# Kernel optimization log

Hardware: AMD Instinct MI355X
Metric: run time of the kernel (lower is better)

The kernel has to match this reference:

```python
import jax, jax.numpy as jnp
import numpy as np
import math

N_GRAPHS = 25
NODES_PER = 2000
N = N_GRAPHS * NODES_PER      # 50000 total nodes
E = 800000                    # total edges
D = 128                       # hidden = out_dim
VOCAB = 30                    # node_len
NLAYERS = 4                   # gcn_num_layers


def setup_inputs() -> dict:
    key = jax.random.key(0)
    ks = jax.random.split(key, 16)
    labels = jax.random.randint(ks[0], (N,), 0, VOCAB)
    src = jax.random.randint(ks[1], (E,), 0, N)
    dst = jax.random.randint(ks[2], (E,), 0, N)
    # true permutations per graph (as the torch code assumes)
    perms = jax.vmap(lambda k: jax.random.permutation(k, NODES_PER))(
        jax.random.split(ks[3], N_GRAPHS))
    s = 0.02
    emb = jax.random.normal(ks[4], (VOCAB, D)) * s
    Ws = jax.random.normal(ks[5], (NLAYERS, D, D)) * s
    bs = jnp.zeros((NLAYERS, D))
    # MLPReadout(D, D) with L=2: D -> D//2 -> D//4 -> D
    w1 = jax.random.normal(ks[6], (D, D // 2)) * s
    b1 = jnp.zeros((D // 2,))
    w2 = jax.random.normal(ks[7], (D // 2, D // 4)) * s
    b2 = jnp.zeros((D // 4,))
    w3 = jax.random.normal(ks[8], (D // 4, D)) * s
    b3 = jnp.zeros((D,))
    return {"labels": labels, "src": src, "dst": dst, "perms": perms,
            "emb": emb, "Ws": Ws, "bs": bs,
            "w1": w1, "b1": b1, "w2": w2, "b2": b2, "w3": w3, "b3": b3}


def _pos_encoding(perms):
    # sinusoidal table [NODES_PER, D]; position starts at 1 per the torch code
    pos = (jnp.arange(NODES_PER, dtype=jnp.float32) + 1.0)[:, None]       # [n,1]
    div = jnp.exp(jnp.arange(0, D, 2, dtype=jnp.float32)
                  * (-math.log(10000.0) / D))                              # [D/2]
    ang = pos * div                                                        # [n,D/2]
    table = jnp.stack([jnp.sin(ang), jnp.cos(ang)], axis=-1).reshape(NODES_PER, D)
    # pes[i][perm_i] = table  (scatter rows per graph)
    pe = jax.vmap(lambda p: jnp.zeros((NODES_PER, D), jnp.float32).at[p].set(table))(perms)
    return pe.reshape(N, D)


def reference(labels, src, dst, perms, emb, Ws, bs, w1, b1, w2, b2, w3, b3):
    h = emb[labels]                                   # embedding lookup [N,D]
    h = h + _pos_encoding(perms)

    ones = jnp.ones((E,), jnp.float32)
    deg_out = jnp.maximum(jax.ops.segment_sum(ones, src, num_segments=N), 1.0)
    deg_in = jnp.maximum(jax.ops.segment_sum(ones, dst, num_segments=N), 1.0)
    isq_src = deg_out ** -0.5                         # DGL GraphConv norm='both'
    isq_dst = deg_in ** -0.5

    for l in range(NLAYERS):
        hn = h * isq_src[:, None]
        m = jax.ops.segment_sum(hn[src], dst, num_segments=N)  # gather-scatter
        m = m * isq_dst[:, None]
        out = jax.nn.relu(m @ Ws[l] + bs[l])
        h = out + h                                   # residual (all dims equal)

    # MLPReadout: D -> D//2 -> D//4 -> D
    x = jax.nn.relu(h @ w1 + b1)
    x = jax.nn.relu(x @ w2 + b2)
    return x @ w3 + b3                                # [N, D]
```

## Files before the change

### kernel.cpp

```cpp
#include <hip/hip_runtime.h>

#define N_NODES 50000
#define N_EDGES 800000
#define D 128
#define NLAYERS 4
#define NODES_PER 2000
#define CAP 64
#define NB_BUILD 3125
#define NB_INIT 25000

typedef __attribute__((ext_vector_type(8))) short bf16x8;
typedef __attribute__((ext_vector_type(4))) float f32x4;

__device__ inline unsigned rne16(float f) {
    unsigned u = __float_as_uint(f);
    return (u + 0x7fffu + ((u >> 16) & 1u)) >> 16;
}
__device__ inline unsigned pack_bf2(float a, float b) {
    return rne16(a) | (rne16(b) << 16);
}
__device__ inline float4 bf4_to_f4(uint2 v) {
    float4 r;
    r.x = __uint_as_float(v.x << 16);
    r.y = __uint_as_float(v.x & 0xffff0000u);
    r.z = __uint_as_float(v.y << 16);
    r.w = __uint_as_float(v.y & 0xffff0000u);
    return r;
}

__global__ void build_init_kernel(const int* __restrict__ src, const int* __restrict__ dst,
                                  int* __restrict__ cursor, int* __restrict__ cnt_out_rep,
                                  unsigned short* __restrict__ bucket,
                                  const int* __restrict__ labels, const int* __restrict__ perms,
                                  const float* __restrict__ emb, float* __restrict__ h,
                                  const float* __restrict__ Ws, unsigned short* __restrict__ Wt,
                                  const float* __restrict__ w1, unsigned short* __restrict__ w1t,
                                  const float* __restrict__ w2, unsigned short* __restrict__ w2t,
                                  const float* __restrict__ w3, unsigned short* __restrict__ w3t) {
    int b = blockIdx.x;
    if (b < NB_BUILD) {
        int e = b * 256 + threadIdx.x;
        if (e < N_EDGES) {
            int s = src[e], d = dst[e];
            atomicAdd(&cnt_out_rep[(b & 3) * N_NODES + s], 1);
            int pos = atomicAdd(&cursor[d], 1);
            if (pos < CAP) bucket[d * CAP + pos] = (unsigned short)s;
        }
    } else if (b < NB_BUILD + NB_INIT) {
        int j = (b - NB_BUILD) * 2 + (threadIdx.x >> 7);
        int d = threadIdx.x & 127;
        int g = j / NODES_PER;
        int i = j - g * NODES_PER;
        int node = g * NODES_PER + perms[j];
        int k = d >> 1;
        float ang = (float)(i + 1) * expf((float)(2 * k) * (-9.210340371976184f / 128.0f));
        float pe = (d & 1) ? cosf(ang) : sinf(ang);
        h[node * D + d] = emb[labels[node] * D + d] + pe;
    } else {
        int tb = b - NB_BUILD - NB_INIT;
        if (tb < NLAYERS) {
            const float* W = Ws + (size_t)tb * D * D;
            unsigned short* T = Wt + (size_t)tb * D * D;
            for (int i = threadIdx.x; i < D * D; i += 256) {
                int k = i >> 7, n = i & 127;
                T[n * D + k] = (unsigned short)rne16(W[i]);
            }
        } else if (tb == NLAYERS) {
            for (int i = threadIdx.x; i < 128 * 64; i += 256) {
                int k = i >> 6, n = i & 63;
                w1t[n * 128 + k] = (unsigned short)rne16(w1[i]);
            }
        } else if (tb == NLAYERS + 1) {
            for (int i = threadIdx.x; i < 64 * 32; i += 256) {
                int k = i >> 5, n = i & 31;
                w2t[n * 64 + k] = (unsigned short)rne16(w2[i]);
            }
        } else {
            for (int i = threadIdx.x; i < 32 * 128; i += 256) {
                int k = i >> 7, n = i & 127;
                w3t[n * 32 + k] = (unsigned short)rne16(w3[i]);
            }
        }
    }
}

__global__ void finalize_kernel(const int* __restrict__ cursor,
                                const int* __restrict__ cnt_out_rep,
                                float* __restrict__ isq_src, float* __restrict__ isq_dst) {
    int i = blockIdx.x * 256 + threadIdx.x;
    if (i < N_NODES) {
        int co = cnt_out_rep[i] + cnt_out_rep[N_NODES + i] +
                 cnt_out_rep[2 * N_NODES + i] + cnt_out_rep[3 * N_NODES + i];
        isq_src[i] = rsqrtf((float)max(co, 1));
        isq_dst[i] = rsqrtf((float)max(cursor[i], 1));
    }
}

__global__ void hs16_kernel(const float* __restrict__ h, const float* __restrict__ isq_src,
                            unsigned short* __restrict__ hs16) {
    int gid = blockIdx.x * 256 + threadIdx.x;
    int row = gid >> 4;
    int c8 = (gid & 15) * 8;
    float s = isq_src[row];
    size_t idx = (size_t)row * D + c8;
    float4 v0 = *(const float4*)&h[idx];
    float4 v1 = *(const float4*)&h[idx + 4];
    uint4 o;
    o.x = pack_bf2(v0.x * s, v0.y * s);
    o.y = pack_bf2(v0.z * s, v0.w * s);
    o.z = pack_bf2(v1.x * s, v1.y * s);
    o.w = pack_bf2(v1.z * s, v1.w * s);
    *(uint4*)&hs16[idx] = o;
}

__global__ __launch_bounds__(256) void aggregate_kernel(const unsigned short* __restrict__ hs16,
        const int* __restrict__ cursor, const unsigned short* __restrict__ bucket,
        const float* __restrict__ isq_dst, unsigned short* __restrict__ m16) {
    int node = blockIdx.x * 4 + (threadIdx.x >> 6);
    int lane = threadIdx.x & 63;
    int q = lane >> 4;
    int col = lane & 15;
    int deg = min(cursor[node], CAP);
    int start = node * CAP;
    int end = start + deg;
    const unsigned short* hb = hs16 + col * 8;
    float a[8] = {0.f, 0.f, 0.f, 0.f, 0.f, 0.f, 0.f, 0.f};

    int e = start;
    for (; e + 8 <= end; e += 8) {
        int s0 = bucket[e + q];
        int s1 = bucket[e + 4 + q];
        uint4 v0 = *(const uint4*)&hb[s0 * D];
        uint4 v1 = *(const uint4*)&hb[s1 * D];
        float4 f0 = bf4_to_f4(make_uint2(v0.x, v0.y));
        float4 f1 = bf4_to_f4(make_uint2(v0.z, v0.w));
        float4 f2 = bf4_to_f4(make_uint2(v1.x, v1.y));
        float4 f3 = bf4_to_f4(make_uint2(v1.z, v1.w));
        a[0] += f0.x; a[1] += f0.y; a[2] += f0.z; a[3] += f0.w;
        a[4] += f1.x; a[5] += f1.y; a[6] += f1.z; a[7] += f1.w;
        a[0] += f2.x; a[1] += f2.y; a[2] += f2.z; a[3] += f2.w;
        a[4] += f3.x; a[5] += f3.y; a[6] += f3.z; a[7] += f3.w;
    }
    if (e + 4 <= end) {
        int s0 = bucket[e + q];
        uint4 v0 = *(const uint4*)&hb[s0 * D];
        float4 f0 = bf4_to_f4(make_uint2(v0.x, v0.y));
        float4 f1 = bf4_to_f4(make_uint2(v0.z, v0.w));
        a[0] += f0.x; a[1] += f0.y; a[2] += f0.z; a[3] += f0.w;
        a[4] += f1.x; a[5] += f1.y; a[6] += f1.z; a[7] += f1.w;
        e += 4;
    }
    int r = end - e;
    if (q < r) {
        int s0 = bucket[e + q];
        uint4 v0 = *(const uint4*)&hb[s0 * D];
        float4 f0 = bf4_to_f4(make_uint2(v0.x, v0.y));
        float4 f1 = bf4_to_f4(make_uint2(v0.z, v0.w));
        a[0] += f0.x; a[1] += f0.y; a[2] += f0.z; a[3] += f0.w;
        a[4] += f1.x; a[5] += f1.y; a[6] += f1.z; a[7] += f1.w;
    }
#pragma unroll
    for (int i = 0; i < 8; ++i) {
        a[i] += __shfl_xor(a[i], 16, 64);
        a[i] += __shfl_xor(a[i], 32, 64);
    }
    if (q == 0) {
        float wd = isq_dst[node];
        uint4 o;
        o.x = pack_bf2(a[0] * wd, a[1] * wd);
        o.y = pack_bf2(a[2] * wd, a[3] * wd);
        o.z = pack_bf2(a[4] * wd, a[5] * wd);
        o.w = pack_bf2(a[6] * wd, a[7] * wd);
        *(uint4*)&m16[node * D + col * 8] = o;
    }
}

__global__ __launch_bounds__(256) void layer_mfma_kernel(const unsigned short* __restrict__ m16,
        const unsigned short* __restrict__ Wt, const float* __restrict__ bias,
        float* __restrict__ h, unsigned short* __restrict__ hs16,
        const float* __restrict__ isq) {
    int wave = threadIdx.x >> 6;
    int lane = threadIdx.x & 63;
    int rowbase = blockIdx.x * 64 + wave * 16;
    int col16 = lane & 15;
    int kq8 = (lane >> 4) * 8;

    int arow = min(rowbase + col16, N_NODES - 1);
    bf16x8 afrag[4];
#pragma unroll
    for (int kk = 0; kk < 4; ++kk)
        afrag[kk] = *(const bf16x8*)&m16[(size_t)arow * D + kk * 32 + kq8];

    int orow0 = rowbase + (lane >> 4) * 4;

#pragma unroll 2
    for (int nt = 0; nt < 8; ++nt) {
        int ncol = nt * 16 + col16;
        float bv = bias[ncol];
        f32x4 acc = {bv, bv, bv, bv};
#pragma unroll
        for (int kk = 0; kk < 4; ++kk) {
            bf16x8 bfrag = *(const bf16x8*)&Wt[(size_t)ncol * D + kk * 32 + kq8];
            acc = __builtin_amdgcn_mfma_f32_16x16x32_bf16(afrag[kk], bfrag, acc, 0, 0, 0);
        }
#pragma unroll
        for (int r = 0; r < 4; ++r) {
            int row = orow0 + r;
            if (row < N_NODES) {
                size_t idx = (size_t)row * D + ncol;
                float o = fmaxf(acc[r], 0.f) + h[idx];
                h[idx] = o;
                float s = isq ? isq[row] : 1.0f;
                hs16[idx] = (unsigned short)rne16(o * s);
            }
        }
    }
}

__global__ __launch_bounds__(256) void readout_mfma_kernel(const unsigned short* __restrict__ h16,
        const unsigned short* __restrict__ w1t, const float* __restrict__ b1,
        const unsigned short* __restrict__ w2t, const float* __restrict__ b2,
        const unsigned short* __restrict__ w3t, const float* __restrict__ b3,
        float* __restrict__ out) {
    __shared__ __align__(16) unsigned short y1s[4][16][72];
    __shared__ __align__(16) unsigned short y2s[4][16][40];
    int wave = threadIdx.x >> 6;
    int lane = threadIdx.x & 63;
    int rowbase = blockIdx.x * 64 + wave * 16;
    int c16 = lane & 15;
    int kq8 = (lane >> 4) * 8;
    int rt0 = (lane >> 4) * 4;

    int arow = min(rowbase + c16, N_NODES - 1);
    bf16x8 af[4];
#pragma unroll
    for (int kk = 0; kk < 4; ++kk)
        af[kk] = *(const bf16x8*)&h16[(size_t)arow * D + kk * 32 + kq8];

#pragma unroll
    for (int nt = 0; nt < 4; ++nt) {
        int ncol = nt * 16 + c16;
        float bv = b1[ncol];
        f32x4 acc = {bv, bv, bv, bv};
#pragma unroll
        for (int kk = 0; kk < 4; ++kk) {
            bf16x8 bfrag = *(const bf16x8*)&w1t[(size_t)ncol * 128 + kk * 32 + kq8];
            acc = __builtin_amdgcn_mfma_f32_16x16x32_bf16(af[kk], bfrag, acc, 0, 0, 0);
        }
#pragma unroll
        for (int r = 0; r < 4; ++r)
            y1s[wave][rt0 + r][ncol] = (unsigned short)rne16(fmaxf(acc[r], 0.f));
    }

    bf16x8 a2[2];
#pragma unroll
    for (int kk = 0; kk < 2; ++kk)
        a2[kk] = *(const bf16x8*)&y1s[wave][c16][kk * 32 + kq8];
#pragma unroll
    for (int nt = 0; nt < 2; ++nt) {
        int ncol = nt * 16 + c16;
        float bv = b2[ncol];
        f32x4 acc = {bv, bv, bv, bv};
#pragma unroll
        for (int kk = 0; kk < 2; ++kk) {
            bf16x8 bfrag = *(const bf16x8*)&w2t[(size_t)ncol * 64 + kk * 32 + kq8];
            acc = __builtin_amdgcn_mfma_f32_16x16x32_bf16(a2[kk], bfrag, acc, 0, 0, 0);
        }
#pragma unroll
        for (int r = 0; r < 4; ++r)
            y2s[wave][rt0 + r][ncol] = (unsigned short)rne16(fmaxf(acc[r], 0.f));
    }

    bf16x8 a3 = *(const bf16x8*)&y2s[wave][c16][kq8];
#pragma unroll 2
    for (int nt = 0; nt < 8; ++nt) {
        int ncol = nt * 16 + c16;
        float bv = b3[ncol];
        f32x4 acc = {bv, bv, bv, bv};
        bf16x8 bfrag = *(const bf16x8*)&w3t[(size_t)ncol * 32 + kq8];
        acc = __builtin_amdgcn_mfma_f32_16x16x32_bf16(a3, bfrag, acc, 0, 0, 0);
#pragma unroll
        for (int r = 0; r < 4; ++r) {
            int row = rowbase + rt0 + r;
            if (row < N_NODES) out[(size_t)row * D + ncol] = acc[r];
        }
    }
}

extern "C" void kernel_launch(void* const* d_in, const int* in_sizes, int n_in,
                              void* d_out, int out_size, void* d_ws, size_t ws_size,
                              hipStream_t stream) {
    const int*   labels = (const int*)d_in[0];
    const int*   src    = (const int*)d_in[1];
    const int*   dst    = (const int*)d_in[2];
    const int*   perms  = (const int*)d_in[3];
    const float* emb    = (const float*)d_in[4];
    const float* Ws     = (const float*)d_in[5];
    const float* bs     = (const float*)d_in[6];
    const float* w1     = (const float*)d_in[7];
    const float* b1     = (const float*)d_in[8];
    const float* w2     = (const float*)d_in[9];
    const float* b2     = (const float*)d_in[10];
    const float* w3     = (const float*)d_in[11];
    const float* b3     = (const float*)d_in[12];
    float* out = (float*)d_out;

    char* p = (char*)d_ws;
    auto alloc = [&](size_t bytes) -> char* {
        char* r = p;
        p += (bytes + 255) & ~size_t(255);
        return r;
    };
    float*          h       = (float*)alloc((size_t)N_NODES * D * 4);
    unsigned short* hs16    = (unsigned short*)alloc((size_t)N_NODES * D * 2);
    unsigned short* m16     = (unsigned short*)alloc((size_t)N_NODES * D * 2);
    unsigned short* Wt      = (unsigned short*)alloc((size_t)NLAYERS * D * D * 2);
    unsigned short* w1t     = (unsigned short*)alloc((size_t)64 * 128 * 2);
    unsigned short* w2t     = (unsigned short*)alloc((size_t)32 * 64 * 2);
    unsigned short* w3t     = (unsigned short*)alloc((size_t)128 * 32 * 2);
    float*          isq_src = (float*)alloc((size_t)N_NODES * 4);
    float*          isq_dst = (float*)alloc((size_t)N_NODES * 4);
    int*            cursor  = (int*)alloc((size_t)5 * N_NODES * 4);
    int*            cnt_rep = cursor + N_NODES;
    unsigned short* bucket  = (unsigned short*)alloc((size_t)N_NODES * CAP * 2);

    hipMemsetAsync(cursor, 0, (size_t)5 * N_NODES * 4, stream);
    build_init_kernel<<<NB_BUILD + NB_INIT + NLAYERS + 3, 256, 0, stream>>>(
        src, dst, cursor, cnt_rep, bucket,
        labels, perms, emb, h,
        Ws, Wt, w1, w1t, w2, w2t, w3, w3t);
    finalize_kernel<<<(N_NODES + 255) / 256, 256, 0, stream>>>(cursor, cnt_rep,
                                                               isq_src, isq_dst);
    hs16_kernel<<<3125, 256, 0, stream>>>(h, isq_src, hs16);

    for (int l = 0; l < NLAYERS; ++l) {
        aggregate_kernel<<<N_NODES / 4, 256, 0, stream>>>(hs16, cursor, bucket, isq_dst, m16);
        layer_mfma_kernel<<<(N_NODES + 63) / 64, 256, 0, stream>>>(
            m16, Wt + (size_t)l * D * D, bs + (size_t)l * D, h, hs16,
            (l < NLAYERS - 1) ? isq_src : (const float*)nullptr);
    }
    readout_mfma_kernel<<<(N_NODES + 63) / 64, 256, 0, stream>>>(
        hs16, w1t, b1, w2t, b2, w3t, b3, out);
}
```

Before: 455.3 us.

## Fuse aggregation into layer MFMA kernel and partition edge build by node range

Merges the per-layer gather aggregation and the MFMA linear layer into one kernel. Each wave aggregates 16 nodes into swizzled LDS and then feeds them straight to MFMA, which removes the m16 round trip through global memory and one launch per layer. hs16 is double-buffered so that reads and writes in the same kernel do not race. The edge build now has 8 blocks per 1024-edge chunk, each handling one node range. This is meant to localise atomics per XCD, but it reads every edge 8 times and each wave now processes 16 nodes serially, giving less parallelism per block.

```diff
diff --git a/kernel.cpp b/kernel.cpp
--- a/kernel.cpp
+++ b/kernel.cpp
@@ -6,7 +6,10 @@
 #define NLAYERS 4
 #define NODES_PER 2000
 #define CAP 64
-#define NB_BUILD 3125
+#define NODES_PER_XCD 6250
+#define EDGE_CHUNK 1024
+#define NCHUNK ((N_EDGES + EDGE_CHUNK - 1) / EDGE_CHUNK)
+#define NB_BUILD (NCHUNK * 8)
 #define NB_INIT 25000
 
 typedef __attribute__((ext_vector_type(8))) short bf16x8;
@@ -39,12 +42,28 @@
                                   const float* __restrict__ w3, unsigned short* __restrict__ w3t) {
     int b = blockIdx.x;
     if (b < NB_BUILD) {
-        int e = b * 256 + threadIdx.x;
-        if (e < N_EDGES) {
-            int s = src[e], d = dst[e];
-            atomicAdd(&cnt_out_rep[(b & 3) * N_NODES + s], 1);
-            int pos = atomicAdd(&cursor[d], 1);
-            if (pos < CAP) bucket[d * CAP + pos] = (unsigned short)s;
+        int chunk = b >> 3;
+        int xlo = (b & 7) * NODES_PER_XCD;
+        int e0 = chunk * EDGE_CHUNK + threadIdx.x * 4;
+        if (e0 < N_EDGES) {
+            int4 s4 = *(const int4*)&src[e0];
+            int4 d4 = *(const int4*)&dst[e0];
+            int rep = (chunk & 3) * N_NODES;
+#define BUILD_ONE(S, DV)                                                       \
+            {                                                                  \
+                int s_ = (S), d_ = (DV);                                       \
+                if ((unsigned)(s_ - xlo) < NODES_PER_XCD)                      \
+                    atomicAdd(&cnt_out_rep[rep + s_], 1);                      \
+                if ((unsigned)(d_ - xlo) < NODES_PER_XCD) {                    \
+                    int pos = atomicAdd(&cursor[d_], 1);                       \
+                    if (pos < CAP) bucket[d_ * CAP + pos] = (unsigned short)s_;\
+                }                                                              \
+            }
+            BUILD_ONE(s4.x, d4.x)
+            BUILD_ONE(s4.y, d4.y)
+            BUILD_ONE(s4.z, d4.z)
+            BUILD_ONE(s4.w, d4.w)
+#undef BUILD_ONE
         }
     } else if (b < NB_BUILD + NB_INIT) {
         int j = (b - NB_BUILD) * 2 + (threadIdx.x >> 7);
@@ -113,89 +132,84 @@
     *(uint4*)&hs16[idx] = o;
 }
 
-__global__ __launch_bounds__(256) void aggregate_kernel(const unsigned short* __restrict__ hs16,
+__global__ __launch_bounds__(256) void agg_layer_kernel(const unsigned short* __restrict__ hs_in,
         const int* __restrict__ cursor, const unsigned short* __restrict__ bucket,
-        const float* __restrict__ isq_dst, unsigned short* __restrict__ m16) {
-    int node = blockIdx.x * 4 + (threadIdx.x >> 6);
-    int lane = threadIdx.x & 63;
-    int q = lane >> 4;
-    int col = lane & 15;
-    int deg = min(cursor[node], CAP);
-    int start = node * CAP;
-    int end = start + deg;
-    const unsigned short* hb = hs16 + col * 8;
-    float a[8] = {0.f, 0.f, 0.f, 0.f, 0.f, 0.f, 0.f, 0.f};
-
-    int e = start;
-    for (; e + 8 <= end; e += 8) {
-        int s0 = bucket[e + q];
-        int s1 = bucket[e + 4 + q];
-        uint4 v0 = *(const uint4*)&hb[s0 * D];
-        uint4 v1 = *(const uint4*)&hb[s1 * D];
-        float4 f0 = bf4_to_f4(make_uint2(v0.x, v0.y));
-        float4 f1 = bf4_to_f4(make_uint2(v0.z, v0.w));
-        float4 f2 = bf4_to_f4(make_uint2(v1.x, v1.y));
-        float4 f3 = bf4_to_f4(make_uint2(v1.z, v1.w));
-        a[0] += f0.x; a[1] += f0.y; a[2] += f0.z; a[3] += f0.w;
-        a[4] += f1.x; a[5] += f1.y; a[6] += f1.z; a[7] += f1.w;
-        a[0] += f2.x; a[1] += f2.y; a[2] += f2.z; a[3] += f2.w;
-        a[4] += f3.x; a[5] += f3.y; a[6] += f3.z; a[7] += f3.w;
-    }
-    if (e + 4 <= end) {
-        int s0 = bucket[e + q];
-        uint4 v0 = *(const uint4*)&hb[s0 * D];
-        float4 f0 = bf4_to_f4(make_uint2(v0.x, v0.y));
-        float4 f1 = bf4_to_f4(make_uint2(v0.z, v0.w));
-        a[0] += f0.x; a[1] += f0.y; a[2] += f0.z; a[3] += f0.w;
-        a[4] += f1.x; a[5] += f1.y; a[6] += f1.z; a[7] += f1.w;
-        e += 4;
-    }
-    int r = end - e;
-    if (q < r) {
-        int s0 = bucket[e + q];
-        uint4 v0 = *(const uint4*)&hb[s0 * D];
-        float4 f0 = bf4_to_f4(make_uint2(v0.x, v0.y));
-        float4 f1 = bf4_to_f4(make_uint2(v0.z, v0.w));
-        a[0] += f0.x; a[1] += f0.y; a[2] += f0.z; a[3] += f0.w;
-        a[4] += f1.x; a[5] += f1.y; a[6] += f1.z; a[7] += f1.w;
-    }
-#pragma unroll
-    for (int i = 0; i < 8; ++i) {
-        a[i] += __shfl_xor(a[i], 16, 64);
-        a[i] += __shfl_xor(a[i], 32, 64);
-    }
-    if (q == 0) {
-        float wd = isq_dst[node];
-        uint4 o;
-        o.x = pack_bf2(a[0] * wd, a[1] * wd);
-        o.y = pack_bf2(a[2] * wd, a[3] * wd);
-        o.z = pack_bf2(a[4] * wd, a[5] * wd);
-        o.w = pack_bf2(a[6] * wd, a[7] * wd);
-        *(uint4*)&m16[node * D + col * 8] = o;
-    }
-}
-
-__global__ __launch_bounds__(256) void layer_mfma_kernel(const unsigned short* __restrict__ m16,
-        const unsigned short* __restrict__ Wt, const float* __restrict__ bias,
-        float* __restrict__ h, unsigned short* __restrict__ hs16,
-        const float* __restrict__ isq) {
+        const float* __restrict__ isq_dst, const unsigned short* __restrict__ Wt,
+        const float* __restrict__ bias, float* __restrict__ h,
+        unsigned short* __restrict__ hs_out, const float* __restrict__ isq) {
+    __shared__ __align__(16) unsigned short mlds[4][16 * 128];
     int wave = threadIdx.x >> 6;
     int lane = threadIdx.x & 63;
     int rowbase = blockIdx.x * 64 + wave * 16;
-    int col16 = lane & 15;
+    int q = lane >> 4;
+    int col = lane & 15;
+    unsigned short* ml = mlds[wave];
+    const unsigned short* hb = hs_in + col * 8;
+
+    for (int r = 0; r < 16; ++r) {
+        int node = min(rowbase + r, N_NODES - 1);
+        int deg = min(cursor[node], CAP);
+        int start = node * CAP;
+        int end = start + deg;
+        float a[8] = {0.f, 0.f, 0.f, 0.f, 0.f, 0.f, 0.f, 0.f};
+        int e = start;
+        for (; e + 8 <= end; e += 8) {
+            int s0 = bucket[e + q];
+            int s1 = bucket[e + 4 + q];
+            uint4 v0 = *(const uint4*)&hb[s0 * D];
+            uint4 v1 = *(const uint4*)&hb[s1 * D];
+            float4 f0 = bf4_to_f4(make_uint2(v0.x, v0.y));
+            float4 f1 = bf4_to_f4(make_uint2(v0.z, v0.w));
+            float4 f2 = bf4_to_f4(make_uint2(v1.x, v1.y));
+            float4 f3 = bf4_to_f4(make_uint2(v1.z, v1.w));
+            a[0] += f0.x; a[1] += f0.y; a[2] += f0.z; a[3] += f0.w;
+            a[4] += f1.x; a[5] += f1.y; a[6] += f1.z; a[7] += f1.w;
+            a[0] += f2.x; a[1] += f2.y; a[2] += f2.z; a[3] += f2.w;
+            a[4] += f3.x; a[5] += f3.y; a[6] += f3.z; a[7] += f3.w;
+        }
+        if (e + 4 <= end) {
+            int s0 = bucket[e + q];
+            uint4 v0 = *(const uint4*)&hb[s0 * D];
+            float4 f0 = bf4_to_f4(make_uint2(v0.x, v0.y));
+            float4 f1 = bf4_to_f4(make_uint2(v0.z, v0.w));
+            a[0] += f0.x; a[1] += f0.y; a[2] += f0.z; a[3] += f0.w;
+            a[4] += f1.x; a[5] += f1.y; a[6] += f1.z; a[7] += f1.w;
+            e += 4;
+        }
+        if (q < end - e) {
+            int s0 = bucket[e + q];
+            uint4 v0 = *(const uint4*)&hb[s0 * D];
+            float4 f0 = bf4_to_f4(make_uint2(v0.x, v0.y));
+            float4 f1 = bf4_to_f4(make_uint2(v0.z, v0.w));
+            a[0] += f0.x; a[1] += f0.y; a[2] += f0.z; a[3] += f0.w;
+            a[4] += f1.x; a[5] += f1.y; a[6] += f1.z; a[7] += f1.w;
+        }
+#pragma unroll
+        for (int i = 0; i < 8; ++i) {
+            a[i] += __shfl_xor(a[i], 16, 64);
+            a[i] += __shfl_xor(a[i], 32, 64);
+        }
+        if (q == 0) {
+            float wd = isq_dst[node];
+            uint4 o;
+            o.x = pack_bf2(a[0] * wd, a[1] * wd);
+            o.y = pack_bf2(a[2] * wd, a[3] * wd);
+            o.z = pack_bf2(a[4] * wd, a[5] * wd);
+            o.w = pack_bf2(a[6] * wd, a[7] * wd);
+            *(uint4*)&ml[r * 128 + ((col * 8) ^ ((r & 7) << 3))] = o;
+        }
+    }
+    int c16 = lane & 15;
     int kq8 = (lane >> 4) * 8;
-
-    int arow = min(rowbase + col16, N_NODES - 1);
     bf16x8 afrag[4];
 #pragma unroll
     for (int kk = 0; kk < 4; ++kk)
-        afrag[kk] = *(const bf16x8*)&m16[(size_t)arow * D + kk * 32 + kq8];
+        afrag[kk] = *(const bf16x8*)&ml[c16 * 128 + ((kk * 32 + kq8) ^ ((c16 & 7) << 3))];
 
     int orow0 = rowbase + (lane >> 4) * 4;
-
 #pragma unroll 2
     for (int nt = 0; nt < 8; ++nt) {
-        int ncol = nt * 16 + col16;
+        int ncol = nt * 16 + c16;
         float bv = bias[ncol];
         f32x4 acc = {bv, bv, bv, bv};
 #pragma unroll
@@ -211,7 +225,7 @@
                 float o = fmaxf(acc[r], 0.f) + h[idx];
                 h[idx] = o;
                 float s = isq ? isq[row] : 1.0f;
-                hs16[idx] = (unsigned short)rne16(o * s);
+                hs_out[idx] = (unsigned short)rne16(o * s);
             }
         }
     }
@@ -312,8 +326,8 @@
         return r;
     };
     float*          h       = (float*)alloc((size_t)N_NODES * D * 4);
-    unsigned short* hs16    = (unsigned short*)alloc((size_t)N_NODES * D * 2);
-    unsigned short* m16     = (unsigned short*)alloc((size_t)N_NODES * D * 2);
+    unsigned short* hs16a   = (unsigned short*)alloc((size_t)N_NODES * D * 2);
+    unsigned short* hs16b   = (unsigned short*)alloc((size_t)N_NODES * D * 2);
     unsigned short* Wt      = (unsigned short*)alloc((size_t)NLAYERS * D * D * 2);
     unsigned short* w1t     = (unsigned short*)alloc((size_t)64 * 128 * 2);
     unsigned short* w2t     = (unsigned short*)alloc((size_t)32 * 64 * 2);
@@ -331,14 +345,16 @@
         Ws, Wt, w1, w1t, w2, w2t, w3, w3t);
     finalize_kernel<<<(N_NODES + 255) / 256, 256, 0, stream>>>(cursor, cnt_rep,
                                                                isq_src, isq_dst);
-    hs16_kernel<<<3125, 256, 0, stream>>>(h, isq_src, hs16);
-
+    hs16_kernel<<<3125, 256, 0, stream>>>(h, isq_src, hs16a);
+
+    unsigned short* hin = hs16a;
+    unsigned short* hout = hs16b;
     for (int l = 0; l < NLAYERS; ++l) {
-        aggregate_kernel<<<N_NODES / 4, 256, 0, stream>>>(hs16, cursor, bucket, isq_dst, m16);
-        layer_mfma_kernel<<<(N_NODES + 63) / 64, 256, 0, stream>>>(
-            m16, Wt + (size_t)l * D * D, bs + (size_t)l * D, h, hs16,
-            (l < NLAYERS - 1) ? isq_src : (const float*)nullptr);
+        agg_layer_kernel<<<(N_NODES + 63) / 64, 256, 0, stream>>>(
+            hin, cursor, bucket, isq_dst, Wt + (size_t)l * D * D, bs + (size_t)l * D,
+            h, hout, (l < NLAYERS - 1) ? isq_src : (const float*)nullptr);
+        unsigned short* tmp = hin; hin = hout; hout = tmp;
     }
     readout_mfma_kernel<<<(N_NODES + 63) / 64, 256, 0, stream>>>(
-        hs16, w1t, b1, w2t, b2, w3t, b3, out);
-}
+        hin, w1t, b1, w2t, b2, w3t, b3, out);
+}
```

New measurement: 507.4 us. 11.5% more time.

## Fuse feature init with bf16 scaling, vectorize edge build, unroll aggregation

Applied to the files above, without the earlier changes.

Moves the embedding plus positional-encoding initialization out of the build kernel into a separate kernel that also writes the scaled bf16 copy, which removes the standalone hs16 pass and one re-read of h. The edge-build blocks now process four edges per thread using int4 loads. The aggregation loop is unrolled to 16 edges per iteration so more gathers are in flight at once. The trade-off is that init can no longer overlap with the build blocks in one launch, and the init kernel writes bf16 as scalar 2-byte stores.

```diff
diff --git a/kernel.cpp b/kernel.cpp
--- a/kernel.cpp
+++ b/kernel.cpp
@@ -6,8 +6,7 @@
 #define NLAYERS 4
 #define NODES_PER 2000
 #define CAP 64
-#define NB_BUILD 3125
-#define NB_INIT 25000
+#define NB_BUILD 782
 
 typedef __attribute__((ext_vector_type(8))) short bf16x8;
 typedef __attribute__((ext_vector_type(4))) float f32x4;
@@ -28,36 +27,35 @@
     return r;
 }
 
-__global__ void build_init_kernel(const int* __restrict__ src, const int* __restrict__ dst,
-                                  int* __restrict__ cursor, int* __restrict__ cnt_out_rep,
-                                  unsigned short* __restrict__ bucket,
-                                  const int* __restrict__ labels, const int* __restrict__ perms,
-                                  const float* __restrict__ emb, float* __restrict__ h,
-                                  const float* __restrict__ Ws, unsigned short* __restrict__ Wt,
-                                  const float* __restrict__ w1, unsigned short* __restrict__ w1t,
-                                  const float* __restrict__ w2, unsigned short* __restrict__ w2t,
-                                  const float* __restrict__ w3, unsigned short* __restrict__ w3t) {
+__global__ void build_kernel(const int* __restrict__ src, const int* __restrict__ dst,
+                             int* __restrict__ cursor, int* __restrict__ cnt_out_rep,
+                             unsigned short* __restrict__ bucket,
+                             const float* __restrict__ Ws, unsigned short* __restrict__ Wt,
+                             const float* __restrict__ w1, unsigned short* __restrict__ w1t,
+                             const float* __restrict__ w2, unsigned short* __restrict__ w2t,
+                             const float* __restrict__ w3, unsigned short* __restrict__ w3t) {
     int b = blockIdx.x;
     if (b < NB_BUILD) {
-        int e = b * 256 + threadIdx.x;
-        if (e < N_EDGES) {
-            int s = src[e], d = dst[e];
-            atomicAdd(&cnt_out_rep[(b & 3) * N_NODES + s], 1);
-            int pos = atomicAdd(&cursor[d], 1);
-            if (pos < CAP) bucket[d * CAP + pos] = (unsigned short)s;
-        }
-    } else if (b < NB_BUILD + NB_INIT) {
-        int j = (b - NB_BUILD) * 2 + (threadIdx.x >> 7);
-        int d = threadIdx.x & 127;
-        int g = j / NODES_PER;
-        int i = j - g * NODES_PER;
-        int node = g * NODES_PER + perms[j];
-        int k = d >> 1;
-        float ang = (float)(i + 1) * expf((float)(2 * k) * (-9.210340371976184f / 128.0f));
-        float pe = (d & 1) ? cosf(ang) : sinf(ang);
-        h[node * D + d] = emb[labels[node] * D + d] + pe;
+        int e0 = (b * 256 + threadIdx.x) * 4;
+        if (e0 < N_EDGES) {
+            int4 s4 = *(const int4*)&src[e0];
+            int4 d4 = *(const int4*)&dst[e0];
+            int rep = (b & 3) * N_NODES;
+#define BUILD_ONE(S, DV)                                                       \
+            {                                                                  \
+                int s_ = (S), d_ = (DV);                                       \
+                atomicAdd(&cnt_out_rep[rep + s_], 1);                          \
+                int pos = atomicAdd(&cursor[d_], 1);                           \
+                if (pos < CAP) bucket[d_ * CAP + pos] = (unsigned short)s_;    \
+            }
+            BUILD_ONE(s4.x, d4.x)
+            BUILD_ONE(s4.y, d4.y)
+            BUILD_ONE(s4.z, d4.z)
+            BUILD_ONE(s4.w, d4.w)
+#undef BUILD_ONE
+        }
     } else {
-        int tb = b - NB_BUILD - NB_INIT;
+        int tb = b - NB_BUILD;
         if (tb < NLAYERS) {
             const float* W = Ws + (size_t)tb * D * D;
             unsigned short* T = Wt + (size_t)tb * D * D;
@@ -96,21 +94,20 @@
     }
 }
 
-__global__ void hs16_kernel(const float* __restrict__ h, const float* __restrict__ isq_src,
-                            unsigned short* __restrict__ hs16) {
-    int gid = blockIdx.x * 256 + threadIdx.x;
-    int row = gid >> 4;
-    int c8 = (gid & 15) * 8;
-    float s = isq_src[row];
-    size_t idx = (size_t)row * D + c8;
-    float4 v0 = *(const float4*)&h[idx];
-    float4 v1 = *(const float4*)&h[idx + 4];
-    uint4 o;
-    o.x = pack_bf2(v0.x * s, v0.y * s);
-    o.y = pack_bf2(v0.z * s, v0.w * s);
-    o.z = pack_bf2(v1.x * s, v1.y * s);
-    o.w = pack_bf2(v1.z * s, v1.w * s);
-    *(uint4*)&hs16[idx] = o;
+__global__ void init_h_kernel(const int* __restrict__ labels, const int* __restrict__ perms,
+                              const float* __restrict__ emb, const float* __restrict__ isq_src,
+                              float* __restrict__ h, unsigned short* __restrict__ hs16) {
+    int j = blockIdx.x * 2 + (threadIdx.x >> 7);
+    int d = threadIdx.x & 127;
+    int g = j / NODES_PER;
+    int i = j - g * NODES_PER;
+    int node = g * NODES_PER + perms[j];
+    int k = d >> 1;
+    float ang = (float)(i + 1) * expf((float)(2 * k) * (-9.210340371976184f / 128.0f));
+    float pe = (d & 1) ? cosf(ang) : sinf(ang);
+    float v = emb[labels[node] * D + d] + pe;
+    h[node * D + d] = v;
+    hs16[node * D + d] = (unsigned short)rne16(v * isq_src[node]);
 }
 
 __global__ __launch_bounds__(256) void aggregate_kernel(const unsigned short* __restrict__ hs16,
@@ -126,39 +123,45 @@
     const unsigned short* hb = hs16 + col * 8;
     float a[8] = {0.f, 0.f, 0.f, 0.f, 0.f, 0.f, 0.f, 0.f};
 
+#define ACC16(V)                                                   \
+    {                                                              \
+        float4 f0 = bf4_to_f4(make_uint2((V).x, (V).y));           \
+        float4 f1 = bf4_to_f4(make_uint2((V).z, (V).w));           \
+        a[0] += f0.x; a[1] += f0.y; a[2] += f0.z; a[3] += f0.w;    \
+        a[4] += f1.x; a[5] += f1.y; a[6] += f1.z; a[7] += f1.w;    \
+    }
     int e = start;
-    for (; e + 8 <= end; e += 8) {
+    for (; e + 16 <= end; e += 16) {
+        int s0 = bucket[e + q];
+        int s1 = bucket[e + 4 + q];
+        int s2 = bucket[e + 8 + q];
+        int s3 = bucket[e + 12 + q];
+        uint4 v0 = *(const uint4*)&hb[s0 * D];
+        uint4 v1 = *(const uint4*)&hb[s1 * D];
+        uint4 v2 = *(const uint4*)&hb[s2 * D];
+        uint4 v3 = *(const uint4*)&hb[s3 * D];
+        ACC16(v0) ACC16(v1) ACC16(v2) ACC16(v3)
+    }
+    if (e + 8 <= end) {
         int s0 = bucket[e + q];
         int s1 = bucket[e + 4 + q];
         uint4 v0 = *(const uint4*)&hb[s0 * D];
         uint4 v1 = *(const uint4*)&hb[s1 * D];
-        float4 f0 = bf4_to_f4(make_uint2(v0.x, v0.y));
-        float4 f1 = bf4_to_f4(make_uint2(v0.z, v0.w));
-        float4 f2 = bf4_to_f4(make_uint2(v1.x, v1.y));
-        float4 f3 = bf4_to_f4(make_uint2(v1.z, v1.w));
-        a[0] += f0.x; a[1] += f0.y; a[2] += f0.z; a[3] += f0.w;
-        a[4] += f1.x; a[5] += f1.y; a[6] += f1.z; a[7] += f1.w;
-        a[0] += f2.x; a[1] += f2.y; a[2] += f2.z; a[3] += f2.w;
-        a[4] += f3.x; a[5] += f3.y; a[6] += f3.z; a[7] += f3.w;
+        ACC16(v0) ACC16(v1)
+        e += 8;
     }
     if (e + 4 <= end) {
         int s0 = bucket[e + q];
         uint4 v0 = *(const uint4*)&hb[s0 * D];
-        float4 f0 = bf4_to_f4(make_uint2(v0.x, v0.y));
-        float4 f1 = bf4_to_f4(make_uint2(v0.z, v0.w));
-        a[0] += f0.x; a[1] += f0.y; a[2] += f0.z; a[3] += f0.w;
-        a[4] += f1.x; a[5] += f1.y; a[6] += f1.z; a[7] += f1.w;
+        ACC16(v0)
         e += 4;
     }
-    int r = end - e;
-    if (q < r) {
+    if (q < end - e) {
         int s0 = bucket[e + q];
         uint4 v0 = *(const uint4*)&hb[s0 * D];
-        float4 f0 = bf4_to_f4(make_uint2(v0.x, v0.y));
-        float4 f1 = bf4_to_f4(make_uint2(v0.z, v0.w));
-        a[0] += f0.x; a[1] += f0.y; a[2] += f0.z; a[3] += f0.w;
-        a[4] += f1.x; a[5] += f1.y; a[6] += f1.z; a[7] += f1.w;
-    }
+        ACC16(v0)
+    }
+#undef ACC16
 #pragma unroll
     for (int i = 0; i < 8; ++i) {
         a[i] += __shfl_xor(a[i], 16, 64);
@@ -325,13 +328,12 @@
     unsigned short* bucket  = (unsigned short*)alloc((size_t)N_NODES * CAP * 2);
 
     hipMemsetAsync(cursor, 0, (size_t)5 * N_NODES * 4, stream);
-    build_init_kernel<<<NB_BUILD + NB_INIT + NLAYERS + 3, 256, 0, stream>>>(
+    build_kernel<<<NB_BUILD + NLAYERS + 3, 256, 0, stream>>>(
         src, dst, cursor, cnt_rep, bucket,
-        labels, perms, emb, h,
         Ws, Wt, w1, w1t, w2, w2t, w3, w3t);
     finalize_kernel<<<(N_NODES + 255) / 256, 256, 0, stream>>>(cursor, cnt_rep,
                                                                isq_src, isq_dst);
-    hs16_kernel<<<3125, 256, 0, stream>>>(h, isq_src, hs16);
+    init_h_kernel<<<N_NODES / 2, 256, 0, stream>>>(labels, perms, emb, isq_src, h, hs16);
 
     for (int l = 0; l < NLAYERS; ++l) {
         aggregate_kernel<<<N_NODES / 4, 256, 0, stream>>>(hs16, cursor, bucket, isq_dst, m16);
```

After: 459.6 us. About the same (+0.9%).
